# Kernel optimization log

Hardware: AMD Instinct MI355X
Metric: run time of the kernel (lower is better)

## Reference

```python
import jax, jax.numpy as jnp
import numpy as np

B, EMBED, H, W = 16, 256, 64, 64
HEADS, POINTS = 8, 4  # mmcv MultiScaleDeformableAttention defaults, num_levels=1


def make_pe(d, h, w):
    # LoFTR-style PositionEncodingSine: pe[0::4]=sin(x*div), pe[1::4]=cos(x*div),
    # pe[2::4]=sin(y*div), pe[3::4]=cos(y*div); x,y are 1-based cumsum positions.
    y = jnp.broadcast_to(jnp.arange(1, h + 1, dtype=jnp.float32)[:, None], (h, w))
    x = jnp.broadcast_to(jnp.arange(1, w + 1, dtype=jnp.float32)[None, :], (h, w))
    div = jnp.exp(jnp.arange(0, d // 2, 2, dtype=jnp.float32) * (-np.log(10000.0) / (d // 2)))
    div = div[:, None, None]  # (d//4,1,1)
    pe = jnp.stack([jnp.sin(x * div), jnp.cos(x * div), jnp.sin(y * div), jnp.cos(y * div)], axis=1)
    return pe.reshape(d, h, w)[None]  # (1,d,h,w)


def reference_points(h, w):
    # Faithful to original: meshgrid(linspace(0,1,W), linspace(0,1,H), indexing='ij'),
    # stack (col, row), flatten -> (W*H, 2)
    gx, gy = jnp.meshgrid(jnp.linspace(0.0, 1.0, w), jnp.linspace(0.0, 1.0, h), indexing='ij')
    return jnp.stack([gy, gx], -1).reshape(-1, 2)


def reference(query, value, W_off, b_off, W_attn, b_attn, W_val, b_val, W_out, b_out):
    Bq, C, h, w = query.shape
    N = h * w
    d = C // HEADS
    pe = make_pe(C, h, w)
    q = query + pe  # query += self.pe(query)
    q_flat = q.reshape(Bq, C, N).transpose(0, 2, 1)      # (B,N,C)
    v_flat = value.reshape(Bq, C, N).transpose(0, 2, 1)  # (B,N,C)
    # value projection, split heads: (B,heads,N,d) -- spatial index n = y*w + x
    v = (v_flat @ W_val.T + b_val).reshape(Bq, N, HEADS, d).transpose(0, 2, 1, 3)
    off = (q_flat @ W_off.T + b_off).reshape(Bq, N, HEADS, POINTS, 2)
    attn = jax.nn.softmax((q_flat @ W_attn.T + b_attn).reshape(Bq, N, HEADS, POINTS), axis=-1)
    ref = reference_points(h, w)                          # (N,2)
    normalizer = jnp.array([w, h], jnp.float32)           # (W, H) per mmcv
    loc = ref[None, :, None, None, :] + off / normalizer  # (B,N,heads,P,2) in [0,1]
    grid = 2.0 * loc - 1.0                                # grid_sample coords, align_corners=False
    sx = grid[..., 0].transpose(0, 2, 1, 3).reshape(Bq, HEADS, N * POINTS)
    sy = grid[..., 1].transpose(0, 2, 1, 3).reshape(Bq, HEADS, N * POINTS)
    ix = (sx + 1.0) * w * 0.5 - 0.5
    iy = (sy + 1.0) * h * 0.5 - 0.5
    x0f = jnp.floor(ix); y0f = jnp.floor(iy)
    wx = ix - x0f; wy = iy - y0f
    x0 = x0f.astype(jnp.int32); y0 = y0f.astype(jnp.int32)

    def gather(yi, xi):
        # zero padding outside the image
        valid = (xi >= 0) & (xi < w) & (yi >= 0) & (yi < h)
        idx = jnp.clip(yi, 0, h - 1) * w + jnp.clip(xi, 0, w - 1)  # (B,heads,M)
        g = jnp.take_along_axis(v, idx[..., None], axis=2)          # (B,heads,M,d)
        return g * valid[..., None]

    samp = (((1 - wx) * (1 - wy))[..., None] * gather(y0, x0)
            + (wx * (1 - wy))[..., None] * gather(y0, x0 + 1)
            + ((1 - wx) * wy)[..., None] * gather(y0 + 1, x0)
            + (wx * wy)[..., None] * gather(y0 + 1, x0 + 1))        # (B,heads,N*P,d)
    samp = samp.reshape(Bq, HEADS, N, POINTS, d)
    attn_t = attn.transpose(0, 2, 1, 3)                             # (B,heads,N,P)
    out = jnp.einsum('bhnp,bhnpd->bnhd', attn_t, samp).reshape(Bq, N, C)
    out = out @ W_out.T + b_out + q_flat  # mmcv internal identity residual (dropout in eval = id)
    out = out.transpose(0, 2, 1).reshape(Bq, C, h, w)
    return out + q  # outer residual: output + query (query already has pe added)


def setup_inputs():
    key = jax.random.key(0)
    ks = jax.random.split(key, 8)
    s = 0.02
    return {
        'query': jax.random.normal(ks[0], (B, EMBED, H, W), jnp.float32),
        'value': jax.random.normal(ks[1], (B, EMBED, H, W), jnp.float32),
        'W_off': jax.random.normal(ks[2], (HEADS * POINTS * 2, EMBED), jnp.float32) * s,
        'b_off': jax.random.normal(ks[3], (HEADS * POINTS * 2,), jnp.float32) * 2.0,
        'W_attn': jax.random.normal(ks[4], (HEADS * POINTS, EMBED), jnp.float32) * s,
        'b_attn': jnp.zeros((HEADS * POINTS,), jnp.float32),
        'W_val': jax.random.normal(ks[5], (EMBED, EMBED), jnp.float32) * s,
        'b_val': jnp.zeros((EMBED,), jnp.float32),
        'W_out': jax.random.normal(ks[6], (EMBED, EMBED), jnp.float32) * s,
        'b_out': jnp.zeros((EMBED,), jnp.float32),
    }
```

## Files before the change

### kernel.cpp

```cpp
#include <hip/hip_runtime.h>
#include <hip/hip_bf16.h>

typedef __bf16 bf16;
typedef bf16 bf16x8 __attribute__((ext_vector_type(8)));
typedef bf16 bf16x4 __attribute__((ext_vector_type(4)));
typedef float f32x4 __attribute__((ext_vector_type(4)));

#define CB 16
#define CC 256
#define CH 64
#define CW 64
#define CN 4096
#define NHEADS 8
#define NPOINTS 4
#define HDIM 32
#define TBP 129

#define MFMA16(a, b, c) __builtin_amdgcn_mfma_f32_16x16x32_bf16(a, b, c, 0, 0, 0)

__global__ __launch_bounds__(256) void pe_kernel(float* __restrict__ pe) {
    int idx = blockIdx.x * 256 + threadIdx.x;
    if (idx >= CC * CN) return;
    int c = idx >> 12, n = idx & (CN - 1);
    int r = n >> 6, x = n & 63;
    int i = c >> 2, t = c & 3;
    float div = __expf(-logf(10000.0f) * (float)i / 64.0f);
    float arg = ((t < 2) ? (float)(x + 1) : (float)(r + 1)) * div;
    pe[idx] = (t & 1) ? cosf(arg) : sinf(arg);
}

__global__ __launch_bounds__(256) void pack_w(const float* __restrict__ Wv,
                                              const float* __restrict__ Woff,
                                              const float* __restrict__ Wattn,
                                              const float* __restrict__ Wout,
                                              bf16* __restrict__ Wv_bf,
                                              bf16* __restrict__ W96_bf,
                                              bf16* __restrict__ Wout_bf) {
    int i = blockIdx.x * 256 + threadIdx.x;
    if (i < CC * CC) {
        Wv_bf[i] = (bf16)Wv[i];
        Wout_bf[i] = (bf16)Wout[i];
    }
    if (i < 96 * CC) {
        W96_bf[i] = (bf16)((i < 64 * CC) ? Woff[i] : Wattn[i - 64 * CC]);
    }
}

__global__ __launch_bounds__(512) void vproj_f(const float* __restrict__ value,
                                               const bf16* __restrict__ Wv,
                                               const float* __restrict__ bv,
                                               bf16* __restrict__ v_s) {
    __shared__ __align__(16) char smem[17408];
    float* T = (float*)smem;
    const int TP = 66;

    int tid = threadIdx.x, lane = tid & 63, wave = tid >> 6;
    int wm = wave >> 1, wn = wave & 1, g = lane >> 4, lr = lane & 15;
    int n0 = blockIdx.x * 64, b = blockIdx.z;
    int nl = tid & 63, kg = tid >> 6;
    const float* src = value + (size_t)b * CC * CN + n0 + nl;

    float v[8];
#pragma unroll
    for (int p = 0; p < 8; ++p) v[p] = src[(size_t)(kg * 8 + p) * CN];

    f32x4 acc[4][2] = {};
    for (int t = 0; t < 4; ++t) {
        bf16x8 o;
#pragma unroll
        for (int p = 0; p < 8; ++p) o[p] = (bf16)v[p];
        *(bf16x8*)(smem + (t & 1) * 8192 + nl * 128 + ((kg ^ (nl & 7)) * 16)) = o;
        __syncthreads();
        if (t < 3) {
#pragma unroll
            for (int p = 0; p < 8; ++p) v[p] = src[(size_t)((t + 1) * 64 + kg * 8 + p) * CN];
        }
#pragma unroll
        for (int ks = 0; ks < 2; ++ks) {
            bf16x8 af[4], bfr[2];
#pragma unroll
            for (int mf = 0; mf < 4; ++mf)
                af[mf] = *(const bf16x8*)&Wv[(size_t)(wm * 64 + mf * 16 + lr) * CC + t * 64 + ks * 32 + g * 8];
#pragma unroll
            for (int nf = 0; nf < 2; ++nf) {
                int row = wn * 32 + nf * 16 + lr;
                bfr[nf] = *(const bf16x8*)(smem + (t & 1) * 8192 + row * 128 + (((ks * 4 + g) ^ (row & 7)) * 16));
            }
#pragma unroll
            for (int mf = 0; mf < 4; ++mf)
#pragma unroll
                for (int nf = 0; nf < 2; ++nf)
                    acc[mf][nf] = MFMA16(af[mf], bfr[nf], acc[mf][nf]);
        }
    }

    int q = tid & 3, n_l = (tid >> 2) & 63, hh = tid >> 8;
#pragma unroll
    for (int pass = 0; pass < 4; ++pass) {
        __syncthreads();
        if (wm == pass) {
#pragma unroll
            for (int mf = 0; mf < 4; ++mf)
#pragma unroll
                for (int nf = 0; nf < 2; ++nf)
#pragma unroll
                    for (int i = 0; i < 4; ++i)
                        T[(mf * 16 + g * 4 + i) * TP + wn * 32 + nf * 16 + lr] = acc[mf][nf][i];
        }
        __syncthreads();
        int head = pass * 2 + hh;
        bf16x8 o;
#pragma unroll
        for (int u = 0; u < 8; ++u)
            o[u] = (bf16)(T[(hh * 32 + q * 8 + u) * TP + n_l] + bv[pass * 64 + hh * 32 + q * 8 + u]);
        *(bf16x8*)&v_s[(((size_t)b * NHEADS + head) * CN + n0 + n_l) * HDIM + q * 8] = o;
    }
}

__global__ __launch_bounds__(256) void offattn_sample(const float* __restrict__ query,
                                                      const float* __restrict__ pe,
                                                      const bf16* __restrict__ W96,
                                                      const float* __restrict__ boff,
                                                      const float* __restrict__ battn,
                                                      const bf16* __restrict__ v_s,
                                                      bf16* __restrict__ s) {
    __shared__ __align__(16) char smem[33024];
    float* ot = (float*)smem;
    unsigned* tbl = (unsigned*)smem;

    int tid = threadIdx.x, lane = tid & 63, wave = tid >> 6;
    int wm = wave >> 1, wn = wave & 1, g = lane >> 4, lr = lane & 15;
    int bx = blockIdx.x, b = blockIdx.z;
    int n0 = bx * 64;
    int nl = tid & 63, kg = tid >> 6;
    const float* qs = query + (size_t)b * CC * CN + n0 + nl;
    const float* ps = pe + n0 + nl;

    float v[16];
#pragma unroll
    for (int p = 0; p < 16; ++p) {
        size_t off = (size_t)(kg * 16 + p) * CN;
        v[p] = qs[off] + ps[off];
    }

    f32x4 acc[3][2] = {};
    for (int t = 0; t < 4; ++t) {
#pragma unroll
        for (int half = 0; half < 2; ++half) {
            bf16x8 o;
#pragma unroll
            for (int p = 0; p < 8; ++p) o[p] = (bf16)v[half * 8 + p];
            int slot = (kg * 2 + half) ^ (nl & 7);
            *(bf16x8*)(smem + (t & 1) * 8192 + nl * 128 + slot * 16) = o;
        }
        __syncthreads();
        if (t < 3) {
#pragma unroll
            for (int p = 0; p < 16; ++p) {
                size_t off = (size_t)((t + 1) * 64 + kg * 16 + p) * CN;
                v[p] = qs[off] + ps[off];
            }
        }
#pragma unroll
        for (int ks = 0; ks < 2; ++ks) {
            bf16x8 af[3], bfr[2];
#pragma unroll
            for (int mf = 0; mf < 3; ++mf)
                af[mf] = *(const bf16x8*)&W96[(size_t)(wm * 48 + mf * 16 + lr) * CC + t * 64 + ks * 32 + g * 8];
#pragma unroll
            for (int nf = 0; nf < 2; ++nf) {
                int row = wn * 32 + nf * 16 + lr;
                bfr[nf] = *(const bf16x8*)(smem + (t & 1) * 8192 + row * 128 + (((ks * 4 + g) ^ (row & 7)) * 16));
            }
#pragma unroll
            for (int mf = 0; mf < 3; ++mf)
#pragma unroll
                for (int nf = 0; nf < 2; ++nf)
                    acc[mf][nf] = MFMA16(af[mf], bfr[nf], acc[mf][nf]);
        }
    }
    __syncthreads();

#pragma unroll
    for (int mf = 0; mf < 3; ++mf) {
#pragma unroll
        for (int i = 0; i < 4; ++i) {
            int j = wm * 48 + mf * 16 + g * 4 + i;
            float bias = (j < 64) ? boff[j] : battn[j - 64];
#pragma unroll
            for (int nf = 0; nf < 2; ++nf) {
                int col = wn * 32 + nf * 16 + lr;
                ot[j * 65 + col] = acc[mf][nf][i] + bias;
            }
        }
    }
    __syncthreads();

    unsigned pk[2][16];
#pragma unroll
    for (int it = 0; it < 2; ++it) {
        int item = it * 256 + tid;
        int inl = item & 63, h = item >> 6;
        float lg0 = ot[(64 + h * 4 + 0) * 65 + inl];
        float lg1 = ot[(64 + h * 4 + 1) * 65 + inl];
        float lg2 = ot[(64 + h * 4 + 2) * 65 + inl];
        float lg3 = ot[(64 + h * 4 + 3) * 65 + inl];
        float m = fmaxf(fmaxf(lg0, lg1), fmaxf(lg2, lg3));
        float e0 = __expf(lg0 - m), e1 = __expf(lg1 - m);
        float e2 = __expf(lg2 - m), e3 = __expf(lg3 - m);
        float inv = 1.0f / (e0 + e1 + e2 + e3);
        float ep[4] = {e0, e1, e2, e3};
#pragma unroll
        for (int p = 0; p < NPOINTS; ++p) {
            float off0 = ot[(h * 8 + p * 2 + 0) * 65 + inl];
            float off1 = ot[(h * 8 + p * 2 + 1) * 65 + inl];
            float ix = (float)inl * (64.0f / 63.0f) + off0 - 0.5f;
            float iy = (float)bx * (64.0f / 63.0f) + off1 - 0.5f;
            float x0f = floorf(ix), y0f = floorf(iy);
            float wx = ix - x0f, wy = iy - y0f;
            int x0 = (int)x0f, y0 = (int)y0f;
            int x1 = x0 + 1, y1 = y0 + 1;
            float vx0 = (x0 >= 0 && x0 < CW) ? 1.f : 0.f;
            float vx1 = (x1 >= 0 && x1 < CW) ? 1.f : 0.f;
            float vy0 = (y0 >= 0 && y0 < CH) ? 1.f : 0.f;
            float vy1 = (y1 >= 0 && y1 < CH) ? 1.f : 0.f;
            int x0c = min(max(x0, 0), CW - 1), x1c = min(max(x1, 0), CW - 1);
            int y0c = min(max(y0, 0), CH - 1), y1c = min(max(y1, 0), CH - 1);
            float a = ep[p] * inv;
            float w00 = a * (1.f - wx) * (1.f - wy) * vx0 * vy0;
            float w01 = a * wx * (1.f - wy) * vx1 * vy0;
            float w10 = a * (1.f - wx) * wy * vx0 * vy1;
            float w11 = a * wx * wy * vx1 * vy1;
            unsigned c00 = (unsigned)(y0c * CW + x0c), c01 = (unsigned)(y0c * CW + x1c);
            unsigned c10 = (unsigned)(y1c * CW + x0c), c11 = (unsigned)(y1c * CW + x1c);
            pk[it][p * 4 + 0] = ((unsigned)__builtin_bit_cast(unsigned short, (_Float16)w00) << 16) | c00;
            pk[it][p * 4 + 1] = ((unsigned)__builtin_bit_cast(unsigned short, (_Float16)w01) << 16) | c01;
            pk[it][p * 4 + 2] = ((unsigned)__builtin_bit_cast(unsigned short, (_Float16)w10) << 16) | c10;
            pk[it][p * 4 + 3] = ((unsigned)__builtin_bit_cast(unsigned short, (_Float16)w11) << 16) | c11;
        }
    }
    __syncthreads();
#pragma unroll
    for (int it = 0; it < 2; ++it) {
        int item = it * 256 + tid;
        int inl = item & 63, h = item >> 6;
        unsigned* dst = tbl + inl * TBP + h * 16;
#pragma unroll
        for (int e = 0; e < 16; ++e) dst[e] = pk[it][e];
    }
    __syncthreads();

    int q = tid & 3, h2 = (tid >> 2) & 7, ng = tid >> 5;
    const bf16* vb = v_s + (((size_t)b * NHEADS + h2) * CN) * HDIM + q * 8;
#pragma unroll
    for (int iter = 0; iter < 8; ++iter) {
        int snl = iter * 8 + ng;
        const unsigned* tb = tbl + snl * TBP + h2 * 16;
        float a0 = 0.f, a1 = 0.f, a2 = 0.f, a3 = 0.f;
        float a4 = 0.f, a5 = 0.f, a6 = 0.f, a7 = 0.f;
#pragma unroll
        for (int e = 0; e < 16; ++e) {
            unsigned u = tb[e];
            float w = (float)__builtin_bit_cast(_Float16, (unsigned short)(u >> 16));
            int cell = (int)(u & 0xFFFu);
            bf16x8 gv = *(const bf16x8*)&vb[cell * HDIM];
            a0 += w * (float)gv[0]; a1 += w * (float)gv[1];
            a2 += w * (float)gv[2]; a3 += w * (float)gv[3];
            a4 += w * (float)gv[4]; a5 += w * (float)gv[5];
            a6 += w * (float)gv[6]; a7 += w * (float)gv[7];
        }
        bf16x8 o;
        o[0] = (bf16)a0; o[1] = (bf16)a1; o[2] = (bf16)a2; o[3] = (bf16)a3;
        o[4] = (bf16)a4; o[5] = (bf16)a5; o[6] = (bf16)a6; o[7] = (bf16)a7;
        *(bf16x8*)&s[((size_t)b * CN + n0 + snl) * CC + h2 * 32 + q * 8] = o;
    }
}

__global__ __launch_bounds__(256) void outproj_v3(const bf16* __restrict__ s_t,
                                                  const bf16* __restrict__ Wout,
                                                  const float* __restrict__ bout,
                                                  const float* __restrict__ query,
                                                  const float* __restrict__ pe,
                                                  float* __restrict__ out) {
    __shared__ __align__(16) char smem[33792];
    float* T = (float*)smem;
    const int TP = 132;

    int tid = threadIdx.x, lane = tid & 63, wave = tid >> 6;
    int wm = wave >> 1, wn = wave & 1, g = lane >> 4, lr = lane & 15;
    int id = blockIdx.x;
    int swz = (id & 7) * 128 + (id >> 3);
    int n0 = (swz & 31) * 128, c0 = ((swz >> 5) & 1) * 128, b = swz >> 6;
    const bf16* sb = s_t + ((size_t)b * CN + n0) * CC;

    f32x4 acc[4][4] = {};
    for (int t = 0; t < 4; ++t) {
        if (t) __syncthreads();
        uint4 ra[4], rw[4];
#pragma unroll
        for (int j = 0; j < 4; ++j) {
            int idx = tid + j * 256, row = idx >> 3, ch = idx & 7;
            ra[j] = *(const uint4*)&sb[(size_t)row * CC + t * 64 + ch * 8];
            rw[j] = *(const uint4*)&Wout[(size_t)(c0 + row) * CC + t * 64 + ch * 8];
        }
#pragma unroll
        for (int j = 0; j < 4; ++j) {
            int idx = tid + j * 256, row = idx >> 3, ch = idx & 7;
            int so = row * 128 + ((ch ^ (row & 7)) * 16);
            *(uint4*)(smem + so) = ra[j];
            *(uint4*)(smem + 16384 + so) = rw[j];
        }
        __syncthreads();
#pragma unroll
        for (int ks = 0; ks < 2; ++ks) {
            bf16x8 af[4], bfr[4];
#pragma unroll
            for (int mf = 0; mf < 4; ++mf) {
                int row = wm * 64 + mf * 16 + lr;
                af[mf] = *(const bf16x8*)(smem + row * 128 + (((ks * 4 + g) ^ (row & 7)) * 16));
            }
#pragma unroll
            for (int nf = 0; nf < 4; ++nf) {
                int row = wn * 64 + nf * 16 + lr;
                bfr[nf] = *(const bf16x8*)(smem + 16384 + row * 128 + (((ks * 4 + g) ^ (row & 7)) * 16));
            }
#pragma unroll
            for (int mf = 0; mf < 4; ++mf)
#pragma unroll
                for (int nf = 0; nf < 4; ++nf)
                    acc[mf][nf] = MFMA16(af[mf], bfr[nf], acc[mf][nf]);
        }
    }
    __syncthreads();

    int lr5 = tid & 31, rq = tid >> 5;
#pragma unroll
    for (int ch = 0; ch < 2; ++ch) {
        if (wn == ch) {
#pragma unroll
            for (int mf = 0; mf < 4; ++mf)
#pragma unroll
                for (int nf = 0; nf < 4; ++nf) {
                    int cl = nf * 16 + lr;
                    int nl = wm * 64 + mf * 16 + g * 4;
                    *(f32x4*)&T[cl * TP + nl] = acc[mf][nf];
                }
        }
        __syncthreads();
#pragma unroll
        for (int pass = 0; pass < 8; ++pass) {
            int cl = pass * 8 + rq;
            int c = c0 + ch * 64 + cl;
            int n = n0 + lr5 * 4;
            f32x4 v = *(const f32x4*)&T[cl * TP + lr5 * 4];
            size_t base = ((size_t)b * CC + c) * CN + n;
            f32x4 q4 = *(const f32x4*)&query[base];
            f32x4 p4 = *(const f32x4*)&pe[(size_t)c * CN + n];
            float bias = bout[c];
#pragma unroll
            for (int j = 0; j < 4; ++j) v[j] = v[j] + bias + 2.0f * (q4[j] + p4[j]);
            *(f32x4*)&out[base] = v;
        }
        __syncthreads();
    }
}

extern "C" void kernel_launch(void* const* d_in, const int* in_sizes, int n_in,
                              void* d_out, int out_size, void* d_ws, size_t ws_size,
                              hipStream_t stream) {
    const float* query = (const float*)d_in[0];
    const float* value = (const float*)d_in[1];
    const float* W_off = (const float*)d_in[2];
    const float* b_off = (const float*)d_in[3];
    const float* W_attn = (const float*)d_in[4];
    const float* b_attn = (const float*)d_in[5];
    const float* W_val = (const float*)d_in[6];
    const float* b_val = (const float*)d_in[7];
    const float* W_out = (const float*)d_in[8];
    const float* b_out = (const float*)d_in[9];
    float* out = (float*)d_out;

    char* p = (char*)d_ws;
    float* pe = (float*)p;            p += (size_t)CC * CN * 4;
    bf16* Wv_bf = (bf16*)p;           p += (size_t)CC * CC * 2;
    bf16* Wout_bf = (bf16*)p;         p += (size_t)CC * CC * 2;
    bf16* W96_bf = (bf16*)p;          p += (size_t)96 * CC * 2 + 256;
    bf16* v_s = (bf16*)p;             p += (size_t)CB * NHEADS * CN * HDIM * 2;
    bf16* s_t = (bf16*)p;             p += (size_t)CB * CN * CC * 2;

    pe_kernel<<<dim3((CC * CN + 255) / 256), dim3(256), 0, stream>>>(pe);
    pack_w<<<dim3(256), dim3(256), 0, stream>>>(W_val, W_off, W_attn, W_out,
                                                Wv_bf, W96_bf, Wout_bf);
    vproj_f<<<dim3(CN / 64, 1, CB), dim3(512), 0, stream>>>(value, Wv_bf, b_val, v_s);
    offattn_sample<<<dim3(CN / 64, 1, CB), dim3(256), 0, stream>>>(query, pe, W96_bf,
                                                                   b_off, b_attn, v_s, s_t);
    outproj_v3<<<dim3(1024), dim3(256), 0, stream>>>(s_t, Wout_bf, b_out, query, pe, out);
}
```

Measured before the change: 159.4 us.

## Batch gathers and vectorize table access in sampler; prefetch tiles in outproj

In the sampling kernel, the lookup table row pitch is padded to 132 so each row is 16-byte aligned. Table entries are now written and read as uint4, and all 16 gathers are issued before the weighted accumulation, which gives more memory-level parallelism. An occupancy hint of 4 blocks per CU is added, and the sampler's shared buffer is enlarged to fit the new pitch. The output projection kernel register-prefetches the next K tile from global memory while the MFMAs run on the current tile; this costs more registers and changes the access pattern to two threads per row.

```diff
diff --git a/kernel.cpp b/kernel.cpp
--- a/kernel.cpp
+++ b/kernel.cpp
@@ -14,7 +14,7 @@
 #define NHEADS 8
 #define NPOINTS 4
 #define HDIM 32
-#define TBP 129
+#define TBP 132
 
 #define MFMA16(a, b, c) __builtin_amdgcn_mfma_f32_16x16x32_bf16(a, b, c, 0, 0, 0)
 
@@ -117,14 +117,14 @@
     }
 }
 
-__global__ __launch_bounds__(256) void offattn_sample(const float* __restrict__ query,
-                                                      const float* __restrict__ pe,
-                                                      const bf16* __restrict__ W96,
-                                                      const float* __restrict__ boff,
-                                                      const float* __restrict__ battn,
-                                                      const bf16* __restrict__ v_s,
-                                                      bf16* __restrict__ s) {
-    __shared__ __align__(16) char smem[33024];
+__global__ __launch_bounds__(256, 4) void offattn_sample(const float* __restrict__ query,
+                                                         const float* __restrict__ pe,
+                                                         const bf16* __restrict__ W96,
+                                                         const float* __restrict__ boff,
+                                                         const float* __restrict__ battn,
+                                                         const bf16* __restrict__ v_s,
+                                                         bf16* __restrict__ s) {
+    __shared__ __align__(16) char smem[33792];
     float* ot = (float*)smem;
     unsigned* tbl = (unsigned*)smem;
 
@@ -244,9 +244,14 @@
     for (int it = 0; it < 2; ++it) {
         int item = it * 256 + tid;
         int inl = item & 63, h = item >> 6;
-        unsigned* dst = tbl + inl * TBP + h * 16;
-#pragma unroll
-        for (int e = 0; e < 16; ++e) dst[e] = pk[it][e];
+        uint4* dst = (uint4*)(tbl + inl * TBP + h * 16);
+#pragma unroll
+        for (int j = 0; j < 4; ++j) {
+            uint4 w4;
+            w4.x = pk[it][j * 4 + 0]; w4.y = pk[it][j * 4 + 1];
+            w4.z = pk[it][j * 4 + 2]; w4.w = pk[it][j * 4 + 3];
+            dst[j] = w4;
+        }
     }
     __syncthreads();
 
@@ -255,19 +260,27 @@
 #pragma unroll
     for (int iter = 0; iter < 8; ++iter) {
         int snl = iter * 8 + ng;
-        const unsigned* tb = tbl + snl * TBP + h2 * 16;
+        const uint4* tb4 = (const uint4*)(tbl + snl * TBP + h2 * 16);
+        unsigned ue[16];
+#pragma unroll
+        for (int j = 0; j < 4; ++j) {
+            uint4 t4 = tb4[j];
+            ue[j * 4 + 0] = t4.x; ue[j * 4 + 1] = t4.y;
+            ue[j * 4 + 2] = t4.z; ue[j * 4 + 3] = t4.w;
+        }
+        bf16x8 gr[16];
+#pragma unroll
+        for (int e = 0; e < 16; ++e)
+            gr[e] = *(const bf16x8*)&vb[(int)(ue[e] & 0xFFFu) * HDIM];
         float a0 = 0.f, a1 = 0.f, a2 = 0.f, a3 = 0.f;
         float a4 = 0.f, a5 = 0.f, a6 = 0.f, a7 = 0.f;
 #pragma unroll
         for (int e = 0; e < 16; ++e) {
-            unsigned u = tb[e];
-            float w = (float)__builtin_bit_cast(_Float16, (unsigned short)(u >> 16));
-            int cell = (int)(u & 0xFFFu);
-            bf16x8 gv = *(const bf16x8*)&vb[cell * HDIM];
-            a0 += w * (float)gv[0]; a1 += w * (float)gv[1];
-            a2 += w * (float)gv[2]; a3 += w * (float)gv[3];
-            a4 += w * (float)gv[4]; a5 += w * (float)gv[5];
-            a6 += w * (float)gv[6]; a7 += w * (float)gv[7];
+            float w = (float)__builtin_bit_cast(_Float16, (unsigned short)(ue[e] >> 16));
+            a0 += w * (float)gr[e][0]; a1 += w * (float)gr[e][1];
+            a2 += w * (float)gr[e][2]; a3 += w * (float)gr[e][3];
+            a4 += w * (float)gr[e][4]; a5 += w * (float)gr[e][5];
+            a6 += w * (float)gr[e][6]; a7 += w * (float)gr[e][7];
         }
         bf16x8 o;
         o[0] = (bf16)a0; o[1] = (bf16)a1; o[2] = (bf16)a2; o[3] = (bf16)a3;
@@ -276,7 +289,7 @@
     }
 }
 
-__global__ __launch_bounds__(256) void outproj_v3(const bf16* __restrict__ s_t,
+__global__ __launch_bounds__(256) void outproj_v4(const bf16* __restrict__ s_t,
                                                   const bf16* __restrict__ Wout,
                                                   const float* __restrict__ bout,
                                                   const float* __restrict__ query,
@@ -293,24 +306,30 @@
     int n0 = (swz & 31) * 128, c0 = ((swz >> 5) & 1) * 128, b = swz >> 6;
     const bf16* sb = s_t + ((size_t)b * CN + n0) * CC;
 
+    int srow = tid >> 1, sch0 = (tid & 1) * 4;
+    uint4 ra[4], rw[4];
+#pragma unroll
+    for (int j = 0; j < 4; ++j) {
+        ra[j] = *(const uint4*)&sb[(size_t)srow * CC + (sch0 + j) * 8];
+        rw[j] = *(const uint4*)&Wout[(size_t)(c0 + srow) * CC + (sch0 + j) * 8];
+    }
+
     f32x4 acc[4][4] = {};
     for (int t = 0; t < 4; ++t) {
-        if (t) __syncthreads();
-        uint4 ra[4], rw[4];
 #pragma unroll
         for (int j = 0; j < 4; ++j) {
-            int idx = tid + j * 256, row = idx >> 3, ch = idx & 7;
-            ra[j] = *(const uint4*)&sb[(size_t)row * CC + t * 64 + ch * 8];
-            rw[j] = *(const uint4*)&Wout[(size_t)(c0 + row) * CC + t * 64 + ch * 8];
-        }
-#pragma unroll
-        for (int j = 0; j < 4; ++j) {
-            int idx = tid + j * 256, row = idx >> 3, ch = idx & 7;
-            int so = row * 128 + ((ch ^ (row & 7)) * 16);
+            int so = srow * 128 + (((sch0 + j) ^ (srow & 7)) * 16);
             *(uint4*)(smem + so) = ra[j];
             *(uint4*)(smem + 16384 + so) = rw[j];
         }
         __syncthreads();
+        if (t < 3) {
+#pragma unroll
+            for (int j = 0; j < 4; ++j) {
+                ra[j] = *(const uint4*)&sb[(size_t)srow * CC + (t + 1) * 64 + (sch0 + j) * 8];
+                rw[j] = *(const uint4*)&Wout[(size_t)(c0 + srow) * CC + (t + 1) * 64 + (sch0 + j) * 8];
+            }
+        }
 #pragma unroll
         for (int ks = 0; ks < 2; ++ks) {
             bf16x8 af[4], bfr[4];
@@ -330,8 +349,8 @@
                 for (int nf = 0; nf < 4; ++nf)
                     acc[mf][nf] = MFMA16(af[mf], bfr[nf], acc[mf][nf]);
         }
-    }
-    __syncthreads();
+        __syncthreads();
+    }
 
     int lr5 = tid & 31, rq = tid >> 5;
 #pragma unroll
@@ -394,5 +413,5 @@
     vproj_f<<<dim3(CN / 64, 1, CB), dim3(512), 0, stream>>>(value, Wv_bf, b_val, v_s);
     offattn_sample<<<dim3(CN / 64, 1, CB), dim3(256), 0, stream>>>(query, pe, W96_bf,
                                                                    b_off, b_attn, v_s, s_t);
-    outproj_v3<<<dim3(1024), dim3(256), 0, stream>>>(s_t, Wout_bf, b_out, query, pe, out);
-}
+    outproj_v4<<<dim3(1024), dim3(256), 0, stream>>>(s_t, Wout_bf, b_out, query, pe, out);
+}
```

New measurement: 182.3 us. 14.4% more time.
